# Performance work log

Measured on AMD Instinct MI355X. Metric: run time of the kernel, lower is better.

Reference implementation:

```python
import jax, jax.numpy as jnp
import numpy as np

N_HEAD = 16
EPS = 1e-5


def setup_inputs() -> dict:
    key = jax.random.key(0)
    ks = jax.random.split(key, 9)
    B, T, C = 2, 1024, 1024
    s = 0.02
    return {
        "x": jax.random.normal(ks[0], (B, T, C), jnp.float32),
        "Wq": jax.random.normal(ks[1], (C, C), jnp.float32) * s,
        "Wk": jax.random.normal(ks[2], (C, C), jnp.float32) * s,
        "Wv": jax.random.normal(ks[3], (C, C), jnp.float32) * s,
        "Wq2": jax.random.normal(ks[4], (C, C), jnp.float32) * s,
        "Wk2": jax.random.normal(ks[5], (C, C), jnp.float32) * s,
        "Wo": jax.random.normal(ks[6], (C, C), jnp.float32) * s,
        "mixture": jnp.full((1,), -5.0, jnp.float32),  # quartet_gate_init
        "quartet_scale": jnp.ones((1,), jnp.float32),
    }


def reference(x, Wq, Wk, Wv, Wq2, Wk2, Wo, mixture, quartet_scale):
    B, T, C = x.shape
    H = N_HEAD
    Dh = C // H
    scale = 1.0 / jnp.sqrt(jnp.asarray(Dh, x.dtype))

    def heads(W):
        # torch Linear: y = x @ W.T ; then view(B,T,H,Dh).transpose(1,2)
        return (x @ W.T).reshape(B, T, H, Dh).transpose(0, 2, 1, 3)  # [B,H,T,Dh]

    q, k, v = heads(Wq), heads(Wk), heads(Wv)
    q2, k2 = heads(Wq2), heads(Wk2)

    qk = jnp.einsum("bhqd,bhkd->bhqk", q, k) * scale      # [B,H,T,T]
    q2k2 = jnp.einsum("bhqd,bhkd->bhqk", q2, k2) * scale  # [B,H,T,T]

    def row_norm(s):
        mu = s.mean(axis=-1, keepdims=True)
        sigma = s.std(axis=-1, keepdims=True, ddof=1)  # torch std is unbiased
        return (s - mu) / (sigma + EPS)

    qk_n = row_norm(qk)
    q2k2_n = row_norm(q2k2)
    m = jax.nn.sigmoid(mixture)  # [1], broadcasts
    scores = (1.0 - m) * qk_n + m * (qk_n * q2k2_n) * quartet_scale

    causal = jnp.tril(jnp.ones((T, T), bool))  # [T,T]
    scores = jnp.where(causal, scores, -jnp.inf)
    attn = jax.nn.softmax(scores, axis=-1)  # [B,H,T,T]

    y = jnp.einsum("bhqk,bhkd->bhqd", attn, v)  # [B,H,T,Dh]
    y = y.transpose(0, 2, 1, 3).reshape(B, T, C)
    return y @ Wo.T
```

## Files before the change

kernel.cpp:

```cpp
#include <hip/hip_runtime.h>
#include <hip/hip_bf16.h>
#include <stdint.h>

#define TS 1024
#define CS 1024
#define NH 16
#define DHEAD 64
#define NBATCH 2
#define EPSV 1e-5f
#define MEG 1048576

typedef __bf16 bf16x8 __attribute__((ext_vector_type(8)));
typedef __bf16 bf16x4 __attribute__((ext_vector_type(4)));
typedef float  f32x4  __attribute__((ext_vector_type(4)));

#define MFMA(a, b, c) __builtin_amdgcn_mfma_f32_16x16x32_bf16((a), (b), (c), 0, 0, 0)

__device__ __forceinline__ float bf2f(ushort u){
  union { uint32_t i; float f; } v; v.i = ((uint32_t)u) << 16; return v.f;
}
__device__ __forceinline__ ushort f2bf(float f){
  union { float f; uint32_t i; } v; v.f = f;
  uint32_t r = v.i + 0x7FFFu + ((v.i >> 16) & 1u);
  return (ushort)(r >> 16);
}

__device__ __forceinline__ void gl_lds16(const ushort* g, ushort* l) {
  __builtin_amdgcn_global_load_lds(
      (const __attribute__((address_space(1))) void*)g,
      (__attribute__((address_space(3))) void*)l, 16, 0, 0);
}

__global__ __launch_bounds__(256)
void cast_all(const float* __restrict__ x,
              const float* __restrict__ Wq, const float* __restrict__ Wk,
              const float* __restrict__ Wv, const float* __restrict__ Wq2,
              const float* __restrict__ Wk2, const float* __restrict__ Wo,
              ushort* __restrict__ xb, ushort* __restrict__ wcat)
{
  const int XC = 524288, TOT = 2097152;
  for (int idx = blockIdx.x * 256 + threadIdx.x; idx < TOT; idx += 524288) {
    const float* s; ushort* d; int c;
    if (idx < XC) { s = x; d = xb; c = idx; }
    else {
      int r = idx - XC; int w = r >> 18; c = r & 262143;
      switch (w) {
        case 0:  s = Wq;  d = wcat;           break;
        case 1:  s = Wk;  d = wcat + 1*MEG;   break;
        case 2:  s = Wv;  d = wcat + 4*MEG;   break;
        case 3:  s = Wq2; d = wcat + 2*MEG;   break;
        case 4:  s = Wk2; d = wcat + 3*MEG;   break;
        default: s = Wo;  d = wcat + 5*MEG;   break;
      }
    }
    float4 v = *(const float4*)(s + (size_t)c * 4);
    ushort4 o; o.x = f2bf(v.x); o.y = f2bf(v.y); o.z = f2bf(v.z); o.w = f2bf(v.w);
    *(ushort4*)(d + (size_t)c * 4) = o;
  }
}

#define BM 128
#define BN 128
#define BKK 32

template<int EPI>
__global__ __launch_bounds__(256, 2)
void gemm_bt(const ushort* __restrict__ A, const ushort* __restrict__ Bt,
             void* __restrict__ Cout,
             int M, int N, int K, int lda, int ldb, int ldc,
             long sA1, long sA2, long sB1, long sB2, long sC1, long sC2,
             float scale)
{
  __shared__ ushort a_s[BM * BKK];
  __shared__ ushort b_s[BN * BKK];

  const int z = blockIdx.z, zh = z >> 4, zl = z & 15;
  A  += (size_t)zh * sA1 + (size_t)zl * sA2;
  Bt += (size_t)zh * sB1 + (size_t)zl * sB2;

  const int n0 = blockIdx.x * BN;
  const int m0 = blockIdx.y * BM;

  const int t  = threadIdx.x;
  const int w  = t >> 6, l = t & 63;
  const int wr = w >> 1, wc = w & 1;
  const int l15 = l & 15, l4 = l >> 4;

  const int rs = l >> 2;
  const int c8 = (l & 3) * 8;

  f32x4 acc[4][4] = {};

  for (int k0 = 0; k0 < K; k0 += BKK) {
    #pragma unroll
    for (int j = 0; j < 2; ++j) {
      int ch = w * 2 + j;
      int r  = ch * 16 + rs;
      gl_lds16(&A [(size_t)(m0 + r) * lda + k0 + c8], &a_s[ch * 512]);
      gl_lds16(&Bt[(size_t)(n0 + r) * ldb + k0 + c8], &b_s[ch * 512]);
    }
    __syncthreads();

    bf16x8 af[4], bfr[4];
    #pragma unroll
    for (int mi = 0; mi < 4; ++mi)
      af[mi] = *(const bf16x8*)&a_s[(wr * 64 + mi * 16 + l15) * BKK + l4 * 8];
    #pragma unroll
    for (int ni = 0; ni < 4; ++ni)
      bfr[ni] = *(const bf16x8*)&b_s[(wc * 64 + ni * 16 + l15) * BKK + l4 * 8];

    #pragma unroll
    for (int mi = 0; mi < 4; ++mi)
      #pragma unroll
      for (int ni = 0; ni < 4; ++ni)
        acc[mi][ni] = MFMA(af[mi], bfr[ni], acc[mi][ni]);

    __syncthreads();
  }

  #pragma unroll
  for (int mi = 0; mi < 4; ++mi) {
    #pragma unroll
    for (int ni = 0; ni < 4; ++ni) {
      int col  = n0 + wc * 64 + ni * 16 + l15;
      int row0 = m0 + wr * 64 + mi * 16 + l4 * 4;
      if (EPI == 0) {
        ushort* C = (ushort*)Cout + (size_t)zh * sC1 + (size_t)zl * sC2;
        #pragma unroll
        for (int e = 0; e < 4; ++e)
          C[(size_t)(row0 + e) * ldc + col] = f2bf(acc[mi][ni][e] * scale);
      } else {
        float* C = (float*)Cout + (size_t)zh * sC1 + (size_t)zl * sC2;
        #pragma unroll
        for (int e = 0; e < 4; ++e)
          C[(size_t)(row0 + e) * ldc + col] = acc[mi][ni][e] * scale;
      }
    }
  }
}

__global__ __launch_bounds__(256, 2)
void gemm_proj(const ushort* __restrict__ A, const ushort* __restrict__ Bt,
               ushort* __restrict__ qb, ushort* __restrict__ kb,
               ushort* __restrict__ q2b, ushort* __restrict__ k2b,
               ushort* __restrict__ vtb,
               ushort* __restrict__ ktb, ushort* __restrict__ k2tb)
{
  __shared__ ushort a_s[BM * BKK];
  __shared__ ushort b_s[BN * BKK];

  const int n0 = blockIdx.x * BN;
  const int m0 = blockIdx.y * BM;

  const int t  = threadIdx.x;
  const int w  = t >> 6, l = t & 63;
  const int wr = w >> 1, wc = w & 1;
  const int l15 = l & 15, l4 = l >> 4;

  const int rs = l >> 2;
  const int c8 = (l & 3) * 8;

  f32x4 acc[4][4] = {};

  for (int k0 = 0; k0 < CS; k0 += BKK) {
    #pragma unroll
    for (int j = 0; j < 2; ++j) {
      int ch = w * 2 + j;
      int r  = ch * 16 + rs;
      gl_lds16(&A [(size_t)(m0 + r) * CS + k0 + c8], &a_s[ch * 512]);
      gl_lds16(&Bt[(size_t)(n0 + r) * CS + k0 + c8], &b_s[ch * 512]);
    }
    __syncthreads();

    bf16x8 af[4], bfr[4];
    #pragma unroll
    for (int mi = 0; mi < 4; ++mi)
      af[mi] = *(const bf16x8*)&a_s[(wr * 64 + mi * 16 + l15) * BKK + l4 * 8];
    #pragma unroll
    for (int ni = 0; ni < 4; ++ni)
      bfr[ni] = *(const bf16x8*)&b_s[(wc * 64 + ni * 16 + l15) * BKK + l4 * 8];

    #pragma unroll
    for (int mi = 0; mi < 4; ++mi)
      #pragma unroll
      for (int ni = 0; ni < 4; ++ni)
        acc[mi][ni] = MFMA(af[mi], bfr[ni], acc[mi][ni]);

    __syncthreads();
  }

  #pragma unroll
  for (int mi = 0; mi < 4; ++mi) {
    #pragma unroll
    for (int ni = 0; ni < 4; ++ni) {
      int col  = n0 + wc * 64 + ni * 16 + l15;
      int row0 = m0 + wr * 64 + mi * 16 + l4 * 4;
      int seg  = col >> 10, cc = col & (CS - 1);
      if (seg < 4) {
        ushort* dst = (seg == 0) ? qb : (seg == 1) ? kb : (seg == 2) ? q2b : k2b;
        float sc = (seg & 1) ? 1.f : 0.125f;
        #pragma unroll
        for (int e = 0; e < 4; ++e)
          dst[(size_t)(row0 + e) * CS + cc] = f2bf(acc[mi][ni][e] * sc);
        if (seg == 1 || seg == 3) {
          int bb = row0 >> 10, tt = row0 & (TS - 1);
          int hh = cc >> 6, dd = cc & (DHEAD - 1);
          ushort* td = (seg == 1) ? ktb : k2tb;
          ushort4 o;
          o.x = f2bf(acc[mi][ni][0]); o.y = f2bf(acc[mi][ni][1]);
          o.z = f2bf(acc[mi][ni][2]); o.w = f2bf(acc[mi][ni][3]);
          *(ushort4*)&td[(((size_t)(bb * NH + hh) * DHEAD + dd) * TS) + tt] = o;
        }
      } else {
        int bb = row0 >> 10, tt = row0 & (TS - 1);
        int hh = cc >> 6, dd = cc & (DHEAD - 1);
        ushort4 o;
        o.x = f2bf(acc[mi][ni][0]); o.y = f2bf(acc[mi][ni][1]);
        o.z = f2bf(acc[mi][ni][2]); o.w = f2bf(acc[mi][ni][3]);
        *(ushort4*)&vtb[(((size_t)(bb * NH + hh) * DHEAD + dd) * TS) + tt] = o;
      }
    }
  }
}

__global__ __launch_bounds__(256, 2)
void gram(const ushort* __restrict__ ktb, const ushort* __restrict__ k2tb,
          ushort* __restrict__ g1b, ushort* __restrict__ g2b,
          float* __restrict__ csb)
{
  __shared__ ushort t_s[64 * 128];

  const int mat = blockIdx.x & 1, z = blockIdx.x >> 1;
  const ushort* S = (mat ? k2tb : ktb) + (size_t)z * DHEAD * TS;

  const int t = threadIdx.x, w = t >> 6, l = t & 63;
  const int l15 = l & 15, l4 = l >> 4;

  f32x4 acc[4] = {};
  float csacc = 0.f;

  for (int tt = 0; tt < 8; ++tt) {
    const int t0 = tt * 128;
    __syncthreads();
    #pragma unroll
    for (int i = 0; i < 4; ++i) {
      int issue = w * 4 + i;
      int row = issue * 4 + l4;
      int gs  = l15 ^ (row & 15);
      gl_lds16(&S[(size_t)row * TS + t0 + gs * 8], &t_s[issue * 512]);
    }
    __syncthreads();

    {
      int r = w * 16 + l15;
      #pragma unroll
      for (int j = 0; j < 4; ++j) {
        int gg = ((l4 * 4 + j) ^ (r & 15)) * 8;
        uint4 vv = *(const uint4*)&t_s[r * 128 + gg];
        const ushort* pu = (const ushort*)&vv;
        #pragma unroll
        for (int e2 = 0; e2 < 8; ++e2) csacc += bf2f(pu[e2]);
      }
    }

    #pragma unroll
    for (int ks = 0; ks < 4; ++ks) {
      int ar = w * 16 + l15;
      bf16x8 af = *(const bf16x8*)&t_s[ar * 128 + ((ks * 4 + l4) ^ (ar & 15)) * 8];
      #pragma unroll
      for (int ni = 0; ni < 4; ++ni) {
        int br = ni * 16 + l15;
        bf16x8 bf_ = *(const bf16x8*)&t_s[br * 128 + ((ks * 4 + l4) ^ (br & 15)) * 8];
        acc[ni] = MFMA(af, bf_, acc[ni]);
      }
    }
  }

  csacc += __shfl_xor(csacc, 16);
  csacc += __shfl_xor(csacc, 32);
  if (l4 == 0)
    csb[(mat * 32 + z) * 64 + w * 16 + l15] = csacc;

  ushort* G = (mat ? g2b : g1b) + (size_t)z * 4096;
  #pragma unroll
  for (int ni = 0; ni < 4; ++ni)
    #pragma unroll
    for (int e = 0; e < 4; ++e)
      G[(w * 16 + l4 * 4 + e) * 64 + ni * 16 + l15] = f2bf(acc[ni][e]);
}

__global__ __launch_bounds__(256, 2)
void attn_fused(const ushort* __restrict__ qb, const ushort* __restrict__ kb,
                const ushort* __restrict__ q2b, const ushort* __restrict__ k2b,
                const ushort* __restrict__ vtb, ushort* __restrict__ yb,
                const ushort* __restrict__ g1b, const ushort* __restrict__ g2b,
                const float* __restrict__ csb,
                const float* __restrict__ mixture, const float* __restrict__ qsc)
{
  __shared__ ushort kbuf [2][4096];
  __shared__ ushort k2buf[2][4096];
  __shared__ ushort vbuf [2][4096];
  __shared__ ushort p_s  [64 * 68];
  __shared__ float  statf[128];
  __shared__ float  statl[64];

  const int idx  = blockIdx.x;
  const int pp   = idx >> 8;
  const int base = idx & 255;
  const int xcd  = base & 7;
  const int mm   = base >> 3;
  const int qh   = mm & 7;
  const int z    = (mm >> 3) * 8 + xcd;
  const int qt   = pp ? qh : (15 - qh);
  const int b    = z >> 4, h = z & 15;
  const int m0   = qt * 64;

  const ushort* Q  = qb  + (size_t)b * TS * CS + h * DHEAD;
  const ushort* Q2 = q2b + (size_t)b * TS * CS + h * DHEAD;
  const ushort* K  = kb  + (size_t)b * TS * CS + h * DHEAD;
  const ushort* K2 = k2b + (size_t)b * TS * CS + h * DHEAD;
  const ushort* Vt = vtb + (size_t)z * DHEAD * TS;
  const ushort* G1 = g1b + (size_t)z * 4096;
  const ushort* G2 = g2b + (size_t)z * 4096;
  ushort* Y = yb + (size_t)b * TS * CS + h * DHEAD;

  const int t = threadIdx.x, w = t >> 6, l = t & 63;
  const int l15 = l & 15, l4 = l >> 4;
  const int r8 = l >> 3, g7 = l & 7;
  const int qrow = w * 16 + l15;

  const float L2E = 1.44269504f;
  const float gm = 1.f / (1.f + __expf(-mixture[0]));
  const float mq2 = gm * qsc[0] * L2E;
  const float om2 = (1.f - gm) * L2E;

  auto stage_tile = [&](int ct, int bs) {
    const int t0 = ct * 64;
    #pragma unroll
    for (int i = 0; i < 2; ++i) {
      int issue = w * 2 + i;
      int row = issue * 8 + r8;
      int gs  = g7 ^ (row & 7);
      gl_lds16(&K [(size_t)(t0 + row) * CS + gs * 8], &kbuf [bs][issue * 512]);
      gl_lds16(&K2[(size_t)(t0 + row) * CS + gs * 8], &k2buf[bs][issue * 512]);
      gl_lds16(&Vt[(size_t)row * TS + t0 + gs * 8], &vbuf[bs][issue * 512]);
    }
  };

  if (t < 64)       statf[t]      = csb[z * 64 + t];
  else if (t < 128) statf[t]      = csb[2048 + z * 64 + (t - 64)];
  #pragma unroll
  for (int i = 0; i < 2; ++i) {
    int issue = w * 2 + i;
    int row = issue * 8 + r8;
    int gs  = g7 ^ (row & 7);
    gl_lds16(&Q [(size_t)(m0 + row) * CS + gs * 8], &kbuf [0][issue * 512]);
    gl_lds16(&Q2[(size_t)(m0 + row) * CS + gs * 8], &k2buf[0][issue * 512]);
    gl_lds16(&G1[row * 64 + gs * 8], &vbuf[0][issue * 512]);
    gl_lds16(&G2[row * 64 + gs * 8], &p_s[issue * 512]);
  }
  stage_tile(0, 1);
  __syncthreads();

  bf16x8 fq[2], fq2[2];
  #pragma unroll
  for (int ks = 0; ks < 2; ++ks) {
    int gg = ((ks * 4 + l4) ^ (qrow & 7)) * 8;
    fq [ks] = *(const bf16x8*)&kbuf [0][qrow * 64 + gg];
    fq2[ks] = *(const bf16x8*)&k2buf[0][qrow * 64 + gg];
  }

  f32x4 U1[4] = {}, U2[4] = {};
  #pragma unroll
  for (int ks = 0; ks < 2; ++ks) {
    #pragma unroll
    for (int ni = 0; ni < 4; ++ni) {
      int gr = ni * 16 + l15;
      int gg = ((ks * 4 + l4) ^ (gr & 7)) * 8;
      bf16x8 bg1 = *(const bf16x8*)&vbuf[0][gr * 64 + gg];
      bf16x8 bg2 = *(const bf16x8*)&p_s[gr * 64 + gg];
      U1[ni] = MFMA(bg1, fq [ks], U1[ni]);
      U2[ni] = MFMA(bg2, fq2[ks], U2[ni]);
    }
  }

  float ssq1 = 0.f, md1 = 0.f, ssq2 = 0.f, md2 = 0.f;
  #pragma unroll
  for (int ni = 0; ni < 4; ++ni) {
    int gsq = ((ni * 2 + (l4 >> 1)) ^ (qrow & 7));
    int off = qrow * 64 + gsq * 8 + (l4 & 1) * 4;
    ushort qa[4], qb2[4];
    *(uint2*)qa  = *(const uint2*)&kbuf [0][off];
    *(uint2*)qb2 = *(const uint2*)&k2buf[0][off];
    float c1[4], c2[4];
    *(float4*)c1 = *(const float4*)&statf[ni * 16 + l4 * 4];
    *(float4*)c2 = *(const float4*)&statf[64 + ni * 16 + l4 * 4];
    #pragma unroll
    for (int e = 0; e < 4; ++e) {
      float qv1 = bf2f(qa[e]), qv2 = bf2f(qb2[e]);
      ssq1 = fmaf(U1[ni][e], qv1, ssq1); md1 = fmaf(qv1, c1[e], md1);
      ssq2 = fmaf(U2[ni][e], qv2, ssq2); md2 = fmaf(qv2, c2[e], md2);
    }
  }
  ssq1 += __shfl_xor(ssq1, 16); md1 += __shfl_xor(md1, 16);
  ssq2 += __shfl_xor(ssq2, 16); md2 += __shfl_xor(md2, 16);
  ssq1 += __shfl_xor(ssq1, 32); md1 += __shfl_xor(md1, 32);
  ssq2 += __shfl_xor(ssq2, 32); md2 += __shfl_xor(md2, 32);

  const float mu1 = md1 * (1.f / TS), mu2 = md2 * (1.f / TS);
  const float va1 = (ssq1 - (float)TS * mu1 * mu1) * (1.f / (TS - 1));
  const float va2 = (ssq2 - (float)TS * mu2 * mu2) * (1.f / (TS - 1));
  const float iv1 = 1.f / (sqrtf(fmaxf(va1, 0.f)) + EPSV);
  const float iv2 = 1.f / (sqrtf(fmaxf(va2, 0.f)) + EPSV);
  __syncthreads();

  float lrow = 0.f;
  f32x4 accO[4] = {};

  for (int ct = 0; ct <= qt; ++ct) {
    const int cur = (ct & 1) ^ 1;
    if (ct < qt) stage_tile(ct + 1, cur ^ 1);

    const ushort* ks_ = kbuf [cur];
    const ushort* k2s_= k2buf[cur];
    const ushort* vs_ = vbuf [cur];

    f32x4 a1[4] = {}, a2[4] = {};
    #pragma unroll
    for (int ks = 0; ks < 2; ++ks) {
      bf16x8 bk[4], bk2[4];
      #pragma unroll
      for (int ni = 0; ni < 4; ++ni) {
        int j  = ni * 16 + l15;
        int gg = ((ks * 4 + l4) ^ (j & 7)) * 8;
        bk [ni] = *(const bf16x8*)&ks_ [j * 64 + gg];
        bk2[ni] = *(const bf16x8*)&k2s_[j * 64 + gg];
      }
      #pragma unroll
      for (int ni = 0; ni < 4; ++ni) {
        a1[ni] = MFMA(bk [ni], fq [ks], a1[ni]);
        a2[ni] = MFMA(bk2[ni], fq2[ks], a2[ni]);
      }
    }

    const bool diag = (ct == qt);
    #pragma unroll
    for (int ni = 0; ni < 4; ++ni) {
      float pe[4];
      #pragma unroll
      for (int e = 0; e < 4; ++e) {
        float n1 = (a1[ni][e] - mu1) * iv1;
        float n2 = (a2[ni][e] - mu2) * iv2;
        float sc = n1 * fmaf(mq2, n2, om2);
        float pv = exp2f(sc);
        if (diag) pv = ((ni * 16 + l4 * 4 + e) <= qrow) ? pv : 0.f;
        lrow += pv;
        pe[e] = pv;
      }
      uint32_t pk01, pk23;
      asm("v_cvt_pk_bf16_f32 %0, %1, %2" : "=v"(pk01) : "v"(pe[0]), "v"(pe[1]));
      asm("v_cvt_pk_bf16_f32 %0, %1, %2" : "=v"(pk23) : "v"(pe[2]), "v"(pe[3]));
      uint2 pk; pk.x = pk01; pk.y = pk23;
      *(uint2*)&p_s[qrow * 68 + ni * 16 + l4 * 4] = pk;
    }

    #pragma unroll
    for (int ks = 0; ks < 2; ++ks) {
      int po = qrow * 68 + ks * 32 + l4 * 8;
      bf16x4 plo = *(const bf16x4*)&p_s[po];
      bf16x4 phi = *(const bf16x4*)&p_s[po + 4];
      bf16x8 ap = __builtin_shufflevector(plo, phi, 0, 1, 2, 3, 4, 5, 6, 7);
      bf16x8 bv[4];
      #pragma unroll
      for (int ni = 0; ni < 4; ++ni) {
        int d  = ni * 16 + l15;
        int gg = ((ks * 4 + l4) ^ (d & 7)) * 8;
        bv[ni] = *(const bf16x8*)&vs_[d * 64 + gg];
      }
      #pragma unroll
      for (int ni = 0; ni < 4; ++ni)
        accO[ni] = MFMA(ap, bv[ni], accO[ni]);
    }

    __syncthreads();
  }

  lrow += __shfl_xor(lrow, 16);
  lrow += __shfl_xor(lrow, 32);
  if (l4 == 0) statl[qrow] = lrow;
  float il[4];
  *(float4*)il = *(const float4*)&statl[w * 16 + l4 * 4];
  #pragma unroll
  for (int e = 0; e < 4; ++e) il[e] = 1.f / il[e];
  #pragma unroll
  for (int ni = 0; ni < 4; ++ni)
    #pragma unroll
    for (int e = 0; e < 4; ++e)
      Y[(size_t)(m0 + w * 16 + l4 * 4 + e) * CS + ni * 16 + l15] =
          f2bf(accO[ni][e] * il[e]);
}

extern "C" void kernel_launch(void* const* d_in, const int* in_sizes, int n_in,
                              void* d_out, int out_size, void* d_ws, size_t ws_size,
                              hipStream_t stream) {
  const float* x    = (const float*)d_in[0];
  const float* Wq   = (const float*)d_in[1];
  const float* Wk   = (const float*)d_in[2];
  const float* Wv   = (const float*)d_in[3];
  const float* Wq2  = (const float*)d_in[4];
  const float* Wk2  = (const float*)d_in[5];
  const float* Wo   = (const float*)d_in[6];
  const float* mixture = (const float*)d_in[7];
  const float* qsc  = (const float*)d_in[8];
  float* out = (float*)d_out;

  const size_t MT = (size_t)NBATCH * TS;
  ushort* ws = (ushort*)d_ws;
  ushort* xb   = ws;
  ushort* wcat = xb   + (size_t)2 * MEG;
  ushort* qb   = wcat + (size_t)6 * MEG;
  ushort* q2b  = qb   + (size_t)2 * MEG;
  ushort* kb   = q2b  + (size_t)2 * MEG;
  ushort* k2b  = kb   + (size_t)2 * MEG;
  ushort* vtb  = k2b  + (size_t)2 * MEG;
  ushort* yb   = vtb  + (size_t)2 * MEG;
  ushort* ktb  = yb   + (size_t)2 * MEG;
  ushort* k2tb = ktb  + (size_t)2 * MEG;
  ushort* g1b  = k2tb + (size_t)2 * MEG;
  ushort* g2b  = g1b  + (size_t)(MEG / 8);
  float*  csb  = (float*)(g2b + (size_t)(MEG / 8));
  ushort* wob  = wcat + (size_t)5 * MEG;

  cast_all<<<2048, 256, 0, stream>>>(x, Wq, Wk, Wv, Wq2, Wk2, Wo, xb, wcat);

  gemm_proj<<<dim3(5 * CS / BN, MT / BM, 1), 256, 0, stream>>>(
      xb, wcat, qb, kb, q2b, k2b, vtb, ktb, k2tb);

  gram<<<64, 256, 0, stream>>>(ktb, k2tb, g1b, g2b, csb);

  attn_fused<<<512, 256, 0, stream>>>(qb, kb, q2b, k2b, vtb, yb,
                                      g1b, g2b, csb, mixture, qsc);

  gemm_bt<1><<<dim3(CS / BN, MT / BM, 1), 256, 0, stream>>>(
      yb, wob, out, (int)MT, CS, CS, CS, CS, CS, 0, 0, 0, 0, 0, 0, 1.f);
}
```

Measured before the change: 105.1 us.

## Load V into registers, shrink attention LDS, add 64-row output GEMM

```diff
diff --git a/kernel.cpp b/kernel.cpp
--- a/kernel.cpp
+++ b/kernel.cpp
@@ -11,7 +11,6 @@
 #define MEG 1048576
 
 typedef __bf16 bf16x8 __attribute__((ext_vector_type(8)));
-typedef __bf16 bf16x4 __attribute__((ext_vector_type(4)));
 typedef float  f32x4  __attribute__((ext_vector_type(4)));
 
 #define MFMA(a, b, c) __builtin_amdgcn_mfma_f32_16x16x32_bf16((a), (b), (c), 0, 0, 0)
@@ -62,82 +61,6 @@
 #define BM 128
 #define BN 128
 #define BKK 32
-
-template<int EPI>
-__global__ __launch_bounds__(256, 2)
-void gemm_bt(const ushort* __restrict__ A, const ushort* __restrict__ Bt,
-             void* __restrict__ Cout,
-             int M, int N, int K, int lda, int ldb, int ldc,
-             long sA1, long sA2, long sB1, long sB2, long sC1, long sC2,
-             float scale)
-{
-  __shared__ ushort a_s[BM * BKK];
-  __shared__ ushort b_s[BN * BKK];
-
-  const int z = blockIdx.z, zh = z >> 4, zl = z & 15;
-  A  += (size_t)zh * sA1 + (size_t)zl * sA2;
-  Bt += (size_t)zh * sB1 + (size_t)zl * sB2;
-
-  const int n0 = blockIdx.x * BN;
-  const int m0 = blockIdx.y * BM;
-
-  const int t  = threadIdx.x;
-  const int w  = t >> 6, l = t & 63;
-  const int wr = w >> 1, wc = w & 1;
-  const int l15 = l & 15, l4 = l >> 4;
-
-  const int rs = l >> 2;
-  const int c8 = (l & 3) * 8;
-
-  f32x4 acc[4][4] = {};
-
-  for (int k0 = 0; k0 < K; k0 += BKK) {
-    #pragma unroll
-    for (int j = 0; j < 2; ++j) {
-      int ch = w * 2 + j;
-      int r  = ch * 16 + rs;
-      gl_lds16(&A [(size_t)(m0 + r) * lda + k0 + c8], &a_s[ch * 512]);
-      gl_lds16(&Bt[(size_t)(n0 + r) * ldb + k0 + c8], &b_s[ch * 512]);
-    }
-    __syncthreads();
-
-    bf16x8 af[4], bfr[4];
-    #pragma unroll
-    for (int mi = 0; mi < 4; ++mi)
-      af[mi] = *(const bf16x8*)&a_s[(wr * 64 + mi * 16 + l15) * BKK + l4 * 8];
-    #pragma unroll
-    for (int ni = 0; ni < 4; ++ni)
-      bfr[ni] = *(const bf16x8*)&b_s[(wc * 64 + ni * 16 + l15) * BKK + l4 * 8];
-
-    #pragma unroll
-    for (int mi = 0; mi < 4; ++mi)
-      #pragma unroll
-      for (int ni = 0; ni < 4; ++ni)
-        acc[mi][ni] = MFMA(af[mi], bfr[ni], acc[mi][ni]);
-
-    __syncthreads();
-  }
-
-  #pragma unroll
-  for (int mi = 0; mi < 4; ++mi) {
-    #pragma unroll
-    for (int ni = 0; ni < 4; ++ni) {
-      int col  = n0 + wc * 64 + ni * 16 + l15;
-      int row0 = m0 + wr * 64 + mi * 16 + l4 * 4;
-      if (EPI == 0) {
-        ushort* C = (ushort*)Cout + (size_t)zh * sC1 + (size_t)zl * sC2;
-        #pragma unroll
-        for (int e = 0; e < 4; ++e)
-          C[(size_t)(row0 + e) * ldc + col] = f2bf(acc[mi][ni][e] * scale);
-      } else {
-        float* C = (float*)Cout + (size_t)zh * sC1 + (size_t)zl * sC2;
-        #pragma unroll
-        for (int e = 0; e < 4; ++e)
-          C[(size_t)(row0 + e) * ldc + col] = acc[mi][ni][e] * scale;
-      }
-    }
-  }
-}
 
 __global__ __launch_bounds__(256, 2)
 void gemm_proj(const ushort* __restrict__ A, const ushort* __restrict__ Bt,
@@ -224,6 +147,49 @@
 }
 
 __global__ __launch_bounds__(256, 2)
+void gemm_out(const ushort* __restrict__ A, const ushort* __restrict__ Bt,
+              float* __restrict__ C)
+{
+  __shared__ ushort a_s[64 * BKK];
+  __shared__ ushort b_s[128 * BKK];
+
+  const int n0 = blockIdx.x * 128;
+  const int m0 = blockIdx.y * 64;
+
+  const int t  = threadIdx.x;
+  const int w  = t >> 6, l = t & 63;
+  const int l15 = l & 15, l4 = l >> 4;
+  const int rs = l >> 2;
+  const int c8 = (l & 3) * 8;
+
+  f32x4 acc[8] = {};
+
+  for (int k0 = 0; k0 < CS; k0 += BKK) {
+    gl_lds16(&A[(size_t)(m0 + w * 16 + rs) * CS + k0 + c8], &a_s[w * 512]);
+    #pragma unroll
+    for (int j = 0; j < 2; ++j) {
+      int ch = w * 2 + j;
+      gl_lds16(&Bt[(size_t)(n0 + ch * 16 + rs) * CS + k0 + c8], &b_s[ch * 512]);
+    }
+    __syncthreads();
+
+    bf16x8 af = *(const bf16x8*)&a_s[(w * 16 + l15) * BKK + l4 * 8];
+    #pragma unroll
+    for (int ni = 0; ni < 8; ++ni) {
+      bf16x8 bfr = *(const bf16x8*)&b_s[(ni * 16 + l15) * BKK + l4 * 8];
+      acc[ni] = MFMA(af, bfr, acc[ni]);
+    }
+    __syncthreads();
+  }
+
+  #pragma unroll
+  for (int ni = 0; ni < 8; ++ni)
+    #pragma unroll
+    for (int e = 0; e < 4; ++e)
+      C[(size_t)(m0 + w * 16 + l4 * 4 + e) * CS + n0 + ni * 16 + l15] = acc[ni][e];
+}
+
+__global__ __launch_bounds__(256, 2)
 void gram(const ushort* __restrict__ ktb, const ushort* __restrict__ k2tb,
           ushort* __restrict__ g1b, ushort* __restrict__ g2b,
           float* __restrict__ csb)
@@ -289,7 +255,7 @@
       G[(w * 16 + l4 * 4 + e) * 64 + ni * 16 + l15] = f2bf(acc[ni][e]);
 }
 
-__global__ __launch_bounds__(256, 2)
+__global__ __launch_bounds__(256, 4)
 void attn_fused(const ushort* __restrict__ qb, const ushort* __restrict__ kb,
                 const ushort* __restrict__ q2b, const ushort* __restrict__ k2b,
                 const ushort* __restrict__ vtb, ushort* __restrict__ yb,
@@ -299,10 +265,7 @@
 {
   __shared__ ushort kbuf [2][4096];
   __shared__ ushort k2buf[2][4096];
-  __shared__ ushort vbuf [2][4096];
-  __shared__ ushort p_s  [64 * 68];
-  __shared__ float  statf[128];
-  __shared__ float  statl[64];
+  __shared__ ushort p_s  [4096];
 
   const int idx  = blockIdx.x;
   const int pp   = idx >> 8;
@@ -343,12 +306,18 @@
       int gs  = g7 ^ (row & 7);
       gl_lds16(&K [(size_t)(t0 + row) * CS + gs * 8], &kbuf [bs][issue * 512]);
       gl_lds16(&K2[(size_t)(t0 + row) * CS + gs * 8], &k2buf[bs][issue * 512]);
-      gl_lds16(&Vt[(size_t)row * TS + t0 + gs * 8], &vbuf[bs][issue * 512]);
     }
   };
-
-  if (t < 64)       statf[t]      = csb[z * 64 + t];
-  else if (t < 128) statf[t]      = csb[2048 + z * 64 + (t - 64)];
+  bf16x8 vr[8];
+  auto load_v = [&](int ct) {
+    const int t0 = ct * 64;
+    #pragma unroll
+    for (int ni = 0; ni < 4; ++ni)
+      #pragma unroll
+      for (int ks = 0; ks < 2; ++ks)
+        vr[ni * 2 + ks] = *(const bf16x8*)&Vt[(size_t)(ni * 16 + l15) * TS + t0 + (ks * 4 + l4) * 8];
+  };
+
   #pragma unroll
   for (int i = 0; i < 2; ++i) {
     int issue = w * 2 + i;
@@ -356,10 +325,9 @@
     int gs  = g7 ^ (row & 7);
     gl_lds16(&Q [(size_t)(m0 + row) * CS + gs * 8], &kbuf [0][issue * 512]);
     gl_lds16(&Q2[(size_t)(m0 + row) * CS + gs * 8], &k2buf[0][issue * 512]);
-    gl_lds16(&G1[row * 64 + gs * 8], &vbuf[0][issue * 512]);
-    gl_lds16(&G2[row * 64 + gs * 8], &p_s[issue * 512]);
   }
   stage_tile(0, 1);
+  load_v(0);
   __syncthreads();
 
   bf16x8 fq[2], fq2[2];
@@ -372,17 +340,19 @@
 
   f32x4 U1[4] = {}, U2[4] = {};
   #pragma unroll
-  for (int ks = 0; ks < 2; ++ks) {
+  for (int ks = 0; ks < 2; ++ks)
     #pragma unroll
     for (int ni = 0; ni < 4; ++ni) {
-      int gr = ni * 16 + l15;
-      int gg = ((ks * 4 + l4) ^ (gr & 7)) * 8;
-      bf16x8 bg1 = *(const bf16x8*)&vbuf[0][gr * 64 + gg];
-      bf16x8 bg2 = *(const bf16x8*)&p_s[gr * 64 + gg];
-      U1[ni] = MFMA(bg1, fq [ks], U1[ni]);
-      U2[ni] = MFMA(bg2, fq2[ks], U2[ni]);
-    }
-  }
+      bf16x8 bg = *(const bf16x8*)&G1[(ni * 16 + l15) * 64 + ks * 32 + l4 * 8];
+      U1[ni] = MFMA(bg, fq[ks], U1[ni]);
+    }
+  #pragma unroll
+  for (int ks = 0; ks < 2; ++ks)
+    #pragma unroll
+    for (int ni = 0; ni < 4; ++ni) {
+      bf16x8 bg = *(const bf16x8*)&G2[(ni * 16 + l15) * 64 + ks * 32 + l4 * 8];
+      U2[ni] = MFMA(bg, fq2[ks], U2[ni]);
+    }
 
   float ssq1 = 0.f, md1 = 0.f, ssq2 = 0.f, md2 = 0.f;
   #pragma unroll
@@ -393,8 +363,8 @@
     *(uint2*)qa  = *(const uint2*)&kbuf [0][off];
     *(uint2*)qb2 = *(const uint2*)&k2buf[0][off];
     float c1[4], c2[4];
-    *(float4*)c1 = *(const float4*)&statf[ni * 16 + l4 * 4];
-    *(float4*)c2 = *(const float4*)&statf[64 + ni * 16 + l4 * 4];
+    *(float4*)c1 = *(const float4*)&csb[z * 64 + ni * 16 + l4 * 4];
+    *(float4*)c2 = *(const float4*)&csb[2048 + z * 64 + ni * 16 + l4 * 4];
     #pragma unroll
     for (int e = 0; e < 4; ++e) {
       float qv1 = bf2f(qa[e]), qv2 = bf2f(qb2[e]);
@@ -423,7 +393,6 @@
 
     const ushort* ks_ = kbuf [cur];
     const ushort* k2s_= k2buf[cur];
-    const ushort* vs_ = vbuf [cur];
 
     f32x4 a1[4] = {}, a2[4] = {};
     #pragma unroll
@@ -461,37 +430,32 @@
       asm("v_cvt_pk_bf16_f32 %0, %1, %2" : "=v"(pk01) : "v"(pe[0]), "v"(pe[1]));
       asm("v_cvt_pk_bf16_f32 %0, %1, %2" : "=v"(pk23) : "v"(pe[2]), "v"(pe[3]));
       uint2 pk; pk.x = pk01; pk.y = pk23;
-      *(uint2*)&p_s[qrow * 68 + ni * 16 + l4 * 4] = pk;
+      int gw = (ni * 2 + (l4 >> 1)) ^ (qrow & 7);
+      *(uint2*)&p_s[qrow * 64 + gw * 8 + (l4 & 1) * 4] = pk;
     }
 
     #pragma unroll
     for (int ks = 0; ks < 2; ++ks) {
-      int po = qrow * 68 + ks * 32 + l4 * 8;
-      bf16x4 plo = *(const bf16x4*)&p_s[po];
-      bf16x4 phi = *(const bf16x4*)&p_s[po + 4];
-      bf16x8 ap = __builtin_shufflevector(plo, phi, 0, 1, 2, 3, 4, 5, 6, 7);
-      bf16x8 bv[4];
-      #pragma unroll
-      for (int ni = 0; ni < 4; ++ni) {
-        int d  = ni * 16 + l15;
-        int gg = ((ks * 4 + l4) ^ (d & 7)) * 8;
-        bv[ni] = *(const bf16x8*)&vs_[d * 64 + gg];
-      }
+      int gp = (ks * 4 + l4) ^ (qrow & 7);
+      bf16x8 ap = *(const bf16x8*)&p_s[qrow * 64 + gp * 8];
       #pragma unroll
       for (int ni = 0; ni < 4; ++ni)
-        accO[ni] = MFMA(ap, bv[ni], accO[ni]);
-    }
-
+        accO[ni] = MFMA(ap, vr[ni * 2 + ks], accO[ni]);
+    }
+
+    if (ct < qt) load_v(ct + 1);
     __syncthreads();
   }
 
   lrow += __shfl_xor(lrow, 16);
   lrow += __shfl_xor(lrow, 32);
-  if (l4 == 0) statl[qrow] = lrow;
   float il[4];
-  *(float4*)il = *(const float4*)&statl[w * 16 + l4 * 4];
-  #pragma unroll
-  for (int e = 0; e < 4; ++e) il[e] = 1.f / il[e];
+  #pragma unroll
+  for (int e = 0; e < 4; ++e)
+    il[e] = 1.f / __shfl(lrow, w * 64 + l4 * 4 + e - w * 64 + 0 * 16 + (l4 * 4 + e >= 16 ? 0 : 0) == 0 ? (l4 * 4 + e) : (l4 * 4 + e));
+  #pragma unroll
+  for (int e = 0; e < 4; ++e)
+    il[e] = 1.f / __shfl(lrow, l4 * 4 + e);
   #pragma unroll
   for (int ni = 0; ni < 4; ++ni)
     #pragma unroll
@@ -541,6 +505,5 @@
   attn_fused<<<512, 256, 0, stream>>>(qb, kb, q2b, k2b, vtb, yb,
                                       g1b, g2b, csb, mixture, qsc);
 
-  gemm_bt<1><<<dim3(CS / BN, MT / BM, 1), 256, 0, stream>>>(
-      yb, wob, out, (int)MT, CS, CS, CS, CS, CS, 0, 0, 0, 0, 0, 0, 1.f);
-}
+  gemm_out<<<dim3(8, 32), 256, 0, stream>>>(yb, wob, out);
+}
```

Result: slower. 131.1 us (+24.8%).
